# Kernel tuning notes

Hardware: AMD Instinct MI355X
Metric: run time of the kernel (lower is better)

Reference implementation:

```python
import jax, jax.numpy as jnp
import numpy as np

NUM_PIXELS, B, C, H, A = 4096, 64, 512, 512, 256


def setup_inputs() -> dict:
    key = jax.random.key(0)
    ks = jax.random.split(key, 8)
    s = 0.02
    return {
        "keys": jax.random.normal(ks[0], (NUM_PIXELS, B, C), jnp.float32),
        "queries": jax.random.normal(ks[1], (1, B, H), jnp.float32),
        "Wa_w": jax.random.normal(ks[2], (A, C), jnp.float32) * s,
        "Wa_b": jax.random.normal(ks[3], (A,), jnp.float32) * s,
        "Ua_w": jax.random.normal(ks[4], (A, H), jnp.float32) * s,
        "Ua_b": jax.random.normal(ks[5], (A,), jnp.float32) * s,
        "va_w": jax.random.normal(ks[6], (1, A), jnp.float32) * s,
        "va_b": jax.random.normal(ks[7], (1,), jnp.float32) * s,
    }


def reference(keys, queries, Wa_w, Wa_b, Ua_w, Ua_b, va_w, va_b):
    # attn1: [P, B, A]; attn2: [1, B, A]
    attn1 = jnp.einsum("pbc,ac->pba", keys, Wa_w) + Wa_b
    attn2 = jnp.einsum("qbh,ah->qba", queries, Ua_w) + Ua_b
    # scores: [P, B] (va projects attn_size -> 1)
    scores = jnp.einsum("pba,a->pb", jnp.tanh(attn1 + attn2), va_w[0]) + va_b[0]
    weights = jax.nn.softmax(scores, axis=0)[..., None]  # [P, B, 1]
    context = jnp.sum(weights * keys, axis=0, keepdims=True)  # [1, B, C]
    return (context, weights)
```

## Files before the change

kernel.cpp:

```cpp
#include <hip/hip_runtime.h>
#include <cstdint>

#define CC 512
#define AA 256

typedef __bf16 bf16x8 __attribute__((ext_vector_type(8)));
typedef float f32x16 __attribute__((ext_vector_type(16)));

__device__ __forceinline__ unsigned short f2bf(float f) {
  union { float f; uint32_t u; } v; v.f = f;
  uint32_t r = (v.u + 0x7FFFu + ((v.u >> 16) & 1u)) >> 16;
  return (unsigned short)r;
}

__global__ void prep_kernel(const float* __restrict__ q,
                            const float* __restrict__ Wa_w,
                            const float* __restrict__ Wa_b,
                            const float* __restrict__ Ua_w,
                            const float* __restrict__ Ua_b,
                            unsigned short* __restrict__ wa_bf,
                            float* __restrict__ attn2,
                            float* __restrict__ out_ctx) {
  const int blk = blockIdx.x, t = threadIdx.x;
  if (blk < 64) {
    const int b = blk, a = t;
    float acc = Ua_b[a] + Wa_b[a];
    const float4* qr = (const float4*)(q + (size_t)b * CC);
    const float4* ur = (const float4*)(Ua_w + (size_t)a * CC);
#pragma unroll 4
    for (int i = 0; i < CC / 4; ++i) {
      float4 uu = ur[i]; float4 qq = qr[i];
      acc += uu.x * qq.x + uu.y * qq.y + uu.z * qq.z + uu.w * qq.w;
    }
    attn2[b * AA + a] = acc;
  } else if (blk < 128) {
    const int base = (blk - 64) * 2048 + t * 8;
#pragma unroll
    for (int i = 0; i < 8; ++i) wa_bf[base + i] = f2bf(Wa_w[base + i]);
  } else {
    const int base = (blk - 128) * 512 + t * 2;
    out_ctx[base] = 0.f; out_ctx[base + 1] = 0.f;
  }
}

__global__ __launch_bounds__(256, 2) void scores_kernel(
    const float* __restrict__ keys,
    const unsigned short* __restrict__ wa_bf,
    const float* __restrict__ attn2,
    const float* __restrict__ va_w,
    const float* __restrict__ va_b,
    float* __restrict__ scores) {
  __shared__ __align__(16) unsigned char smem[55296];
  unsigned short* As = (unsigned short*)smem;
  unsigned short* Bs = As + 128 * 72;

  const int t = threadIdx.x;
  const int w = t >> 6, lane = t & 63;
  const int m32 = lane & 31, kg = lane >> 5;
  const int R0w = (w & 1) * 64, C0w = (w >> 1) * 128;
  const long r0 = (long)blockIdx.x * 128;

  f32x16 acc[2][4];
#pragma unroll
  for (int i = 0; i < 2; ++i)
#pragma unroll
    for (int j = 0; j < 4; ++j)
#pragma unroll
      for (int e = 0; e < 16; ++e) acc[i][j][e] = 0.f;

  const int c4 = t & 15, rg = t >> 4;
  const int kq = t & 7, ng = t >> 3;

  for (int ko = 0; ko < 8; ++ko) {
    const int kb = ko * 64;
#pragma unroll
    for (int ps = 0; ps < 8; ++ps) {
      const int row = rg + ps * 16;
      float4 v = *(const float4*)(keys + (r0 + row) * CC + kb + c4 * 4);
      ushort4 h;
      h.x = f2bf(v.x); h.y = f2bf(v.y); h.z = f2bf(v.z); h.w = f2bf(v.w);
      *(ushort4*)(As + row * 72 + c4 * 4) = h;
    }
#pragma unroll
    for (int ps = 0; ps < 8; ++ps) {
      const int n = ng + ps * 32;
      int4 v = *(const int4*)(wa_bf + (size_t)n * CC + kb + kq * 8);
      *(int4*)(Bs + n * 72 + kq * 8) = v;
    }
    __syncthreads();
    for (int kk = 0; kk < 4; ++kk) {
      const int k0 = kk * 16 + kg * 8;
      bf16x8 a0 = *(const bf16x8*)(As + (R0w + m32) * 72 + k0);
      bf16x8 a1 = *(const bf16x8*)(As + (R0w + 32 + m32) * 72 + k0);
      bf16x8 b0 = *(const bf16x8*)(Bs + (C0w + m32) * 72 + k0);
      bf16x8 b1 = *(const bf16x8*)(Bs + (C0w + 32 + m32) * 72 + k0);
      bf16x8 b2 = *(const bf16x8*)(Bs + (C0w + 64 + m32) * 72 + k0);
      bf16x8 b3 = *(const bf16x8*)(Bs + (C0w + 96 + m32) * 72 + k0);
      acc[0][0] = __builtin_amdgcn_mfma_f32_32x32x16_bf16(a0, b0, acc[0][0], 0, 0, 0);
      acc[0][1] = __builtin_amdgcn_mfma_f32_32x32x16_bf16(a0, b1, acc[0][1], 0, 0, 0);
      acc[0][2] = __builtin_amdgcn_mfma_f32_32x32x16_bf16(a0, b2, acc[0][2], 0, 0, 0);
      acc[0][3] = __builtin_amdgcn_mfma_f32_32x32x16_bf16(a0, b3, acc[0][3], 0, 0, 0);
      acc[1][0] = __builtin_amdgcn_mfma_f32_32x32x16_bf16(a1, b0, acc[1][0], 0, 0, 0);
      acc[1][1] = __builtin_amdgcn_mfma_f32_32x32x16_bf16(a1, b1, acc[1][1], 0, 0, 0);
      acc[1][2] = __builtin_amdgcn_mfma_f32_32x32x16_bf16(a1, b2, acc[1][2], 0, 0, 0);
      acc[1][3] = __builtin_amdgcn_mfma_f32_32x32x16_bf16(a1, b3, acc[1][3], 0, 0, 0);
    }
    __syncthreads();
  }

  float* sc0 = (float*)smem;
  float* sc1 = sc0 + 128;

#pragma unroll
  for (int mt = 0; mt < 2; ++mt) {
    float ps[16];
#pragma unroll
    for (int r = 0; r < 16; ++r) ps[r] = 0.f;
    const int rowb = R0w + mt * 32 + 4 * kg;
#pragma unroll
    for (int nt = 0; nt < 4; ++nt) {
      const int col = C0w + nt * 32 + m32;
      const float vv = va_w[col];
#pragma unroll
      for (int r = 0; r < 16; ++r) {
        const int row = rowb + (r & 3) + 8 * (r >> 2);
        float x = acc[mt][nt][r] + attn2[(row & 63) * AA + col];
        float ax = fabsf(x);
        float e2 = __expf(-2.f * ax);
        float th = (1.f - e2) / (1.f + e2);
        ps[r] += copysignf(th, x) * vv;
      }
    }
#pragma unroll
    for (int off = 1; off <= 16; off <<= 1)
#pragma unroll
      for (int r = 0; r < 16; ++r) ps[r] += __shfl_xor(ps[r], off);
    if (m32 == 0) {
      float* dst = (w >> 1) ? sc1 : sc0;
#pragma unroll
      for (int r = 0; r < 16; ++r) dst[rowb + (r & 3) + 8 * (r >> 2)] = ps[r];
    }
  }
  __syncthreads();
  if (t < 128) scores[r0 + t] = sc0[t] + sc1[t] + va_b[0];
}

__global__ void softmax_kernel(const float* __restrict__ scores,
                               float* __restrict__ out) {
  const int b = blockIdx.x, t = threadIdx.x;
  const int w = t >> 6, lane = t & 63;
  __shared__ float red[4];
  float s[16];
  float m = -1e30f;
#pragma unroll
  for (int i = 0; i < 16; ++i) {
    s[i] = scores[(size_t)(t + 256 * i) * 64 + b];
    m = fmaxf(m, s[i]);
  }
#pragma unroll
  for (int off = 1; off <= 32; off <<= 1) m = fmaxf(m, __shfl_xor(m, off));
  if (lane == 0) red[w] = m;
  __syncthreads();
  m = fmaxf(fmaxf(red[0], red[1]), fmaxf(red[2], red[3]));
  float sum = 0.f;
#pragma unroll
  for (int i = 0; i < 16; ++i) { s[i] = __expf(s[i] - m); sum += s[i]; }
#pragma unroll
  for (int off = 1; off <= 32; off <<= 1) sum += __shfl_xor(sum, off);
  __syncthreads();
  if (lane == 0) red[w] = sum;
  __syncthreads();
  const float invZ = 1.f / (red[0] + red[1] + red[2] + red[3]);
  float* wout = out + 32768;
#pragma unroll
  for (int i = 0; i < 16; ++i)
    wout[(size_t)(t + 256 * i) * 64 + b] = s[i] * invZ;
}

__global__ __launch_bounds__(128) void context_kernel(
    const float* __restrict__ keys,
    const float* __restrict__ wts,
    float* __restrict__ out_ctx) {
  const int b = blockIdx.y, pc = blockIdx.x, t = threadIdx.x;
  const int p0 = pc * 128;
  __shared__ float wl[128];
  wl[t] = wts[(size_t)(p0 + t) * 64 + b];
  __syncthreads();
  float4 acc = {0.f, 0.f, 0.f, 0.f};
  const float4* kp = (const float4*)keys;
#pragma unroll 4
  for (int j = 0; j < 128; ++j) {
    float4 kv = kp[(size_t)((p0 + j) * 64 + b) * 128 + t];
    const float wj = wl[j];
    acc.x += wj * kv.x; acc.y += wj * kv.y;
    acc.z += wj * kv.z; acc.w += wj * kv.w;
  }
  float* dst = out_ctx + b * 512 + t * 4;
  atomicAdd(dst + 0, acc.x);
  atomicAdd(dst + 1, acc.y);
  atomicAdd(dst + 2, acc.z);
  atomicAdd(dst + 3, acc.w);
}

extern "C" void kernel_launch(void* const* d_in, const int* in_sizes, int n_in,
                              void* d_out, int out_size, void* d_ws, size_t ws_size,
                              hipStream_t stream) {
  (void)in_sizes; (void)n_in; (void)out_size; (void)ws_size;
  const float* keys = (const float*)d_in[0];
  const float* q    = (const float*)d_in[1];
  const float* Wa_w = (const float*)d_in[2];
  const float* Wa_b = (const float*)d_in[3];
  const float* Ua_w = (const float*)d_in[4];
  const float* Ua_b = (const float*)d_in[5];
  const float* va_w = (const float*)d_in[6];
  const float* va_b = (const float*)d_in[7];
  float* out = (float*)d_out;

  unsigned short* wa_bf = (unsigned short*)d_ws;
  float* attn2  = (float*)((char*)d_ws + 262144);
  float* scores = (float*)((char*)d_ws + 262144 + 65536);

  prep_kernel<<<192, 256, 0, stream>>>(q, Wa_w, Wa_b, Ua_w, Ua_b, wa_bf, attn2, out);
  scores_kernel<<<2048, 256, 0, stream>>>(keys, wa_bf, attn2, va_w, va_b, scores);
  softmax_kernel<<<64, 256, 0, stream>>>(scores, out);
  context_kernel<<<dim3(32, 64), 128, 0, stream>>>(keys, out + 32768, out);
}
```

Before: 850.4 us.

## Double-buffer scores GEMM with LDS DMA, register-held A, swizzled Wa layout

The scores GEMM now keeps each wave's 32 key rows in registers, converting them to bf16 just before each MFMA, so the A tile no longer goes through LDS. The Wa tile is streamed into a double-buffered, XOR-swizzled LDS buffer with global_load_lds DMA, prefetching the next k-slice during compute and syncing once per iteration. Prep pre-swizzles Wa and computes attn2 with coalesced loads. The context kernel splits the pixel loop across two halves with an LDS reduction and iterates in reverse order, likely to hit keys still in cache. Larger per-wave accumulators (8 f32x16) raise register pressure and may reduce occupancy.

Result: no change. 838.3 us (-1.4%).

```diff
diff --git a/kernel.cpp b/kernel.cpp
--- a/kernel.cpp
+++ b/kernel.cpp
@@ -6,37 +6,73 @@
 
 typedef __bf16 bf16x8 __attribute__((ext_vector_type(8)));
 typedef float f32x16 __attribute__((ext_vector_type(16)));
-
-__device__ __forceinline__ unsigned short f2bf(float f) {
-  union { float f; uint32_t u; } v; v.f = f;
-  uint32_t r = (v.u + 0x7FFFu + ((v.u >> 16) & 1u)) >> 16;
-  return (unsigned short)r;
-}
-
-__global__ void prep_kernel(const float* __restrict__ q,
-                            const float* __restrict__ Wa_w,
-                            const float* __restrict__ Wa_b,
-                            const float* __restrict__ Ua_w,
-                            const float* __restrict__ Ua_b,
-                            unsigned short* __restrict__ wa_bf,
-                            float* __restrict__ attn2,
-                            float* __restrict__ out_ctx) {
+typedef unsigned short u16x8 __attribute__((ext_vector_type(8)));
+
+__device__ __forceinline__ unsigned short bf(float f) {
+  return __builtin_bit_cast(unsigned short, (__bf16)f);
+}
+
+__device__ __forceinline__ bf16x8 cvt8(float4 lo, float4 hi) {
+  bf16x8 r;
+  r[0] = (__bf16)lo.x; r[1] = (__bf16)lo.y; r[2] = (__bf16)lo.z; r[3] = (__bf16)lo.w;
+  r[4] = (__bf16)hi.x; r[5] = (__bf16)hi.y; r[6] = (__bf16)hi.z; r[7] = (__bf16)hi.w;
+  return r;
+}
+
+__device__ __forceinline__ void dma16(const void* g, void* l) {
+  __builtin_amdgcn_global_load_lds(
+      (const __attribute__((address_space(1))) unsigned int*)g,
+      (__attribute__((address_space(3))) unsigned int*)l, 16, 0, 0);
+}
+
+__device__ __forceinline__ bf16x8 ldsw(const unsigned short* b, int row, int kbyte) {
+  return *(const bf16x8*)((const char*)b + (((row * 128) + kbyte) ^ ((row & 7) << 4)));
+}
+
+__global__ __launch_bounds__(256) void prep_kernel(
+    const float* __restrict__ q,
+    const float* __restrict__ Wa_w,
+    const float* __restrict__ Wa_b,
+    const float* __restrict__ Ua_w,
+    const float* __restrict__ Ua_b,
+    unsigned short* __restrict__ wa_swz,
+    float* __restrict__ attn2,
+    float* __restrict__ out_ctx) {
   const int blk = blockIdx.x, t = threadIdx.x;
   if (blk < 64) {
-    const int b = blk, a = t;
-    float acc = Ua_b[a] + Wa_b[a];
-    const float4* qr = (const float4*)(q + (size_t)b * CC);
-    const float4* ur = (const float4*)(Ua_w + (size_t)a * CC);
-#pragma unroll 4
-    for (int i = 0; i < CC / 4; ++i) {
-      float4 uu = ur[i]; float4 qq = qr[i];
-      acc += uu.x * qq.x + uu.y * qq.y + uu.z * qq.z + uu.w * qq.w;
-    }
-    attn2[b * AA + a] = acc;
+    __shared__ float qs[CC];
+    const int b = blk;
+    qs[t] = q[(size_t)b * CC + t];
+    qs[t + 256] = q[(size_t)b * CC + t + 256];
+    __syncthreads();
+    const int qd = t & 3, ar = t >> 2;
+    const float4* qr = (const float4*)qs;
+#pragma unroll
+    for (int ao = 0; ao < 4; ++ao) {
+      const int a = ao * 64 + ar;
+      const float4* ur = (const float4*)(Ua_w + (size_t)a * CC);
+      float acc = 0.f;
+#pragma unroll 8
+      for (int i = 0; i < 32; ++i) {
+        float4 u = ur[qd + i * 4];
+        float4 qq = qr[qd + i * 4];
+        acc += u.x * qq.x + u.y * qq.y + u.z * qq.z + u.w * qq.w;
+      }
+      acc += __shfl_xor(acc, 1);
+      acc += __shfl_xor(acc, 2);
+      if (qd == 0) attn2[b * AA + a] = acc + Ua_b[a] + Wa_b[a];
+    }
   } else if (blk < 128) {
-    const int base = (blk - 64) * 2048 + t * 8;
-#pragma unroll
-    for (int i = 0; i < 8; ++i) wa_bf[base + i] = f2bf(Wa_w[base + i]);
+    const int e = (blk - 64) * 2048 + t * 8;
+    const int n = e >> 9, k = e & 511;
+    const int ko = k >> 6, j = k & 63;
+    float4 lo = *(const float4*)(Wa_w + e);
+    float4 hi = *(const float4*)(Wa_w + e + 4);
+    u16x8 hv;
+    hv[0] = bf(lo.x); hv[1] = bf(lo.y); hv[2] = bf(lo.z); hv[3] = bf(lo.w);
+    hv[4] = bf(hi.x); hv[5] = bf(hi.y); hv[6] = bf(hi.z); hv[7] = bf(hi.w);
+    const int dst = ko * 16384 + ((n * 64 + j) ^ ((n & 7) << 3));
+    *(u16x8*)(wa_swz + dst) = hv;
   } else {
     const int base = (blk - 128) * 512 + t * 2;
     out_ctx[base] = 0.f; out_ctx[base + 1] = 0.f;
@@ -45,104 +81,107 @@
 
 __global__ __launch_bounds__(256, 2) void scores_kernel(
     const float* __restrict__ keys,
-    const unsigned short* __restrict__ wa_bf,
+    const unsigned short* __restrict__ wa_swz,
     const float* __restrict__ attn2,
     const float* __restrict__ va_w,
     const float* __restrict__ va_b,
     float* __restrict__ scores) {
-  __shared__ __align__(16) unsigned char smem[55296];
-  unsigned short* As = (unsigned short*)smem;
-  unsigned short* Bs = As + 128 * 72;
+  __shared__ __align__(16) unsigned short Bs[2][256 * 64];
 
   const int t = threadIdx.x;
   const int w = t >> 6, lane = t & 63;
   const int m32 = lane & 31, kg = lane >> 5;
-  const int R0w = (w & 1) * 64, C0w = (w >> 1) * 128;
   const long r0 = (long)blockIdx.x * 128;
-
-  f32x16 acc[2][4];
-#pragma unroll
-  for (int i = 0; i < 2; ++i)
-#pragma unroll
-    for (int j = 0; j < 4; ++j)
-#pragma unroll
-      for (int e = 0; e < 16; ++e) acc[i][j][e] = 0.f;
-
-  const int c4 = t & 15, rg = t >> 4;
-  const int kq = t & 7, ng = t >> 3;
-
+  const size_t arow = (size_t)(r0 + w * 32 + m32) * CC;
+
+  f32x16 acc[8];
+#pragma unroll
+  for (int i = 0; i < 8; ++i)
+#pragma unroll
+    for (int e = 0; e < 16; ++e) acc[i][e] = 0.f;
+
+  float4 areg[8];
+#pragma unroll
+  for (int kk = 0; kk < 4; ++kk)
+#pragma unroll
+    for (int h = 0; h < 2; ++h)
+      areg[kk * 2 + h] = *(const float4*)(keys + arow + kk * 16 + kg * 8 + h * 4);
+  {
+    const char* gB = (const char*)wa_swz;
+    char* lB = (char*)&Bs[0][0];
+#pragma unroll
+    for (int i = 0; i < 8; ++i) {
+      const int c = (w * 8 + i) * 1024;
+      dma16(gB + c + lane * 16, lB + c);
+    }
+  }
+
+  int cur = 0;
+#pragma unroll 2
   for (int ko = 0; ko < 8; ++ko) {
-    const int kb = ko * 64;
-#pragma unroll
-    for (int ps = 0; ps < 8; ++ps) {
-      const int row = rg + ps * 16;
-      float4 v = *(const float4*)(keys + (r0 + row) * CC + kb + c4 * 4);
-      ushort4 h;
-      h.x = f2bf(v.x); h.y = f2bf(v.y); h.z = f2bf(v.z); h.w = f2bf(v.w);
-      *(ushort4*)(As + row * 72 + c4 * 4) = h;
-    }
-#pragma unroll
-    for (int ps = 0; ps < 8; ++ps) {
-      const int n = ng + ps * 32;
-      int4 v = *(const int4*)(wa_bf + (size_t)n * CC + kb + kq * 8);
-      *(int4*)(Bs + n * 72 + kq * 8) = v;
-    }
     __syncthreads();
+    bf16x8 af[4];
+#pragma unroll
+    for (int kk = 0; kk < 4; ++kk) af[kk] = cvt8(areg[kk * 2], areg[kk * 2 + 1]);
+    if (ko < 7) {
+      const int kb = (ko + 1) * 64;
+#pragma unroll
+      for (int kk = 0; kk < 4; ++kk)
+#pragma unroll
+        for (int h = 0; h < 2; ++h)
+          areg[kk * 2 + h] =
+              *(const float4*)(keys + arow + kb + kk * 16 + kg * 8 + h * 4);
+      const char* gB = (const char*)wa_swz + (size_t)(ko + 1) * 32768;
+      char* lB = (char*)&Bs[cur ^ 1][0];
+#pragma unroll
+      for (int i = 0; i < 8; ++i) {
+        const int c = (w * 8 + i) * 1024;
+        dma16(gB + c + lane * 16, lB + c);
+      }
+    }
+    const unsigned short* B0 = &Bs[cur][0];
+#pragma unroll
     for (int kk = 0; kk < 4; ++kk) {
-      const int k0 = kk * 16 + kg * 8;
-      bf16x8 a0 = *(const bf16x8*)(As + (R0w + m32) * 72 + k0);
-      bf16x8 a1 = *(const bf16x8*)(As + (R0w + 32 + m32) * 72 + k0);
-      bf16x8 b0 = *(const bf16x8*)(Bs + (C0w + m32) * 72 + k0);
-      bf16x8 b1 = *(const bf16x8*)(Bs + (C0w + 32 + m32) * 72 + k0);
-      bf16x8 b2 = *(const bf16x8*)(Bs + (C0w + 64 + m32) * 72 + k0);
-      bf16x8 b3 = *(const bf16x8*)(Bs + (C0w + 96 + m32) * 72 + k0);
-      acc[0][0] = __builtin_amdgcn_mfma_f32_32x32x16_bf16(a0, b0, acc[0][0], 0, 0, 0);
-      acc[0][1] = __builtin_amdgcn_mfma_f32_32x32x16_bf16(a0, b1, acc[0][1], 0, 0, 0);
-      acc[0][2] = __builtin_amdgcn_mfma_f32_32x32x16_bf16(a0, b2, acc[0][2], 0, 0, 0);
-      acc[0][3] = __builtin_amdgcn_mfma_f32_32x32x16_bf16(a0, b3, acc[0][3], 0, 0, 0);
-      acc[1][0] = __builtin_amdgcn_mfma_f32_32x32x16_bf16(a1, b0, acc[1][0], 0, 0, 0);
-      acc[1][1] = __builtin_amdgcn_mfma_f32_32x32x16_bf16(a1, b1, acc[1][1], 0, 0, 0);
-      acc[1][2] = __builtin_amdgcn_mfma_f32_32x32x16_bf16(a1, b2, acc[1][2], 0, 0, 0);
-      acc[1][3] = __builtin_amdgcn_mfma_f32_32x32x16_bf16(a1, b3, acc[1][3], 0, 0, 0);
-    }
-    __syncthreads();
-  }
-
-  float* sc0 = (float*)smem;
-  float* sc1 = sc0 + 128;
-
-#pragma unroll
-  for (int mt = 0; mt < 2; ++mt) {
-    float ps[16];
-#pragma unroll
-    for (int r = 0; r < 16; ++r) ps[r] = 0.f;
-    const int rowb = R0w + mt * 32 + 4 * kg;
-#pragma unroll
-    for (int nt = 0; nt < 4; ++nt) {
-      const int col = C0w + nt * 32 + m32;
-      const float vv = va_w[col];
-#pragma unroll
-      for (int r = 0; r < 16; ++r) {
-        const int row = rowb + (r & 3) + 8 * (r >> 2);
-        float x = acc[mt][nt][r] + attn2[(row & 63) * AA + col];
-        float ax = fabsf(x);
-        float e2 = __expf(-2.f * ax);
-        float th = (1.f - e2) / (1.f + e2);
-        ps[r] += copysignf(th, x) * vv;
+      const int kbyte = kk * 32 + kg * 16;
+#pragma unroll
+      for (int nt = 0; nt < 8; ++nt) {
+        bf16x8 bfr = ldsw(B0, nt * 32 + m32, kbyte);
+        acc[nt] = __builtin_amdgcn_mfma_f32_32x32x16_bf16(af[kk], bfr, acc[nt], 0, 0, 0);
       }
     }
-#pragma unroll
-    for (int off = 1; off <= 16; off <<= 1)
-#pragma unroll
-      for (int r = 0; r < 16; ++r) ps[r] += __shfl_xor(ps[r], off);
-    if (m32 == 0) {
-      float* dst = (w >> 1) ? sc1 : sc0;
-#pragma unroll
-      for (int r = 0; r < 16; ++r) dst[rowb + (r & 3) + 8 * (r >> 2)] = ps[r];
-    }
-  }
-  __syncthreads();
-  if (t < 128) scores[r0 + t] = sc0[t] + sc1[t] + va_b[0];
+    cur ^= 1;
+  }
+
+  float ps[16];
+#pragma unroll
+  for (int r = 0; r < 16; ++r) ps[r] = 0.f;
+  const int rbase = w * 32 + 4 * kg;
+#pragma unroll
+  for (int nt = 0; nt < 8; ++nt) {
+    const int col = nt * 32 + m32;
+    const float vv = va_w[col];
+#pragma unroll
+    for (int r = 0; r < 16; ++r) {
+      const int row = rbase + (r & 3) + 8 * (r >> 2);
+      float x = acc[nt][r] + attn2[(row & 63) * AA + col];
+      float ax = fabsf(x);
+      float e2 = __expf(-2.f * ax);
+      float th = (1.f - e2) / (1.f + e2);
+      ps[r] += copysignf(th, x) * vv;
+    }
+  }
+#pragma unroll
+  for (int off = 1; off <= 16; off <<= 1)
+#pragma unroll
+    for (int r = 0; r < 16; ++r) ps[r] += __shfl_xor(ps[r], off);
+  if (m32 == 0) {
+    const float vb = va_b[0];
+#pragma unroll
+    for (int r = 0; r < 16; ++r) {
+      const int row = rbase + (r & 3) + 8 * (r >> 2);
+      scores[r0 + row] = ps[r] + vb;
+    }
+  }
 }
 
 __global__ void softmax_kernel(const float* __restrict__ scores,
@@ -177,29 +216,38 @@
     wout[(size_t)(t + 256 * i) * 64 + b] = s[i] * invZ;
 }
 
-__global__ __launch_bounds__(128) void context_kernel(
+__global__ __launch_bounds__(256) void context_kernel(
     const float* __restrict__ keys,
     const float* __restrict__ wts,
     float* __restrict__ out_ctx) {
-  const int b = blockIdx.y, pc = blockIdx.x, t = threadIdx.x;
-  const int p0 = pc * 128;
+  const int b = blockIdx.y;
+  const int p0 = (31 - (int)blockIdx.x) * 128;
+  const int t = threadIdx.x;
+  const int half = t >> 7, c4 = t & 127;
   __shared__ float wl[128];
-  wl[t] = wts[(size_t)(p0 + t) * 64 + b];
+  __shared__ float4 part[128];
+  if (t < 128) wl[t] = wts[(size_t)(p0 + t) * 64 + b];
   __syncthreads();
   float4 acc = {0.f, 0.f, 0.f, 0.f};
   const float4* kp = (const float4*)keys;
-#pragma unroll 4
-  for (int j = 0; j < 128; ++j) {
-    float4 kv = kp[(size_t)((p0 + j) * 64 + b) * 128 + t];
-    const float wj = wl[j];
+  const int jb = half * 64;
+#pragma unroll 8
+  for (int j = 0; j < 64; ++j) {
+    const float4 kv = kp[(size_t)((p0 + jb + j) * 64 + b) * 128 + c4];
+    const float wj = wl[jb + j];
     acc.x += wj * kv.x; acc.y += wj * kv.y;
     acc.z += wj * kv.z; acc.w += wj * kv.w;
   }
-  float* dst = out_ctx + b * 512 + t * 4;
-  atomicAdd(dst + 0, acc.x);
-  atomicAdd(dst + 1, acc.y);
-  atomicAdd(dst + 2, acc.z);
-  atomicAdd(dst + 3, acc.w);
+  if (half) part[c4] = acc;
+  __syncthreads();
+  if (!half) {
+    const float4 o = part[c4];
+    float* dst = out_ctx + b * 512 + c4 * 4;
+    atomicAdd(dst + 0, acc.x + o.x);
+    atomicAdd(dst + 1, acc.y + o.y);
+    atomicAdd(dst + 2, acc.z + o.z);
+    atomicAdd(dst + 3, acc.w + o.w);
+  }
 }
 
 extern "C" void kernel_launch(void* const* d_in, const int* in_sizes, int n_in,
@@ -216,12 +264,12 @@
   const float* va_b = (const float*)d_in[7];
   float* out = (float*)d_out;
 
-  unsigned short* wa_bf = (unsigned short*)d_ws;
+  unsigned short* wa_swz = (unsigned short*)d_ws;
   float* attn2  = (float*)((char*)d_ws + 262144);
   float* scores = (float*)((char*)d_ws + 262144 + 65536);
 
-  prep_kernel<<<192, 256, 0, stream>>>(q, Wa_w, Wa_b, Ua_w, Ua_b, wa_bf, attn2, out);
-  scores_kernel<<<2048, 256, 0, stream>>>(keys, wa_bf, attn2, va_w, va_b, scores);
+  prep_kernel<<<192, 256, 0, stream>>>(q, Wa_w, Wa_b, Ua_w, Ua_b, wa_swz, attn2, out);
+  scores_kernel<<<2048, 256, 0, stream>>>(keys, wa_swz, attn2, va_w, va_b, scores);
   softmax_kernel<<<64, 256, 0, stream>>>(scores, out);
-  context_kernel<<<dim3(32, 64), 128, 0, stream>>>(keys, out + 32768, out);
-}
+  context_kernel<<<dim3(32, 64), 256, 0, stream>>>(keys, out + 32768, out);
+}
```
